# Kernel tuning notes

Measured on AMD Instinct MI355X. Metric: run time of the kernel, lower is better.

The kernel has to match this reference:

```python
import jax, jax.numpy as jnp
import numpy as np

L, D_IN, D_OUT, H = 4096, 512, 256, 4
HEAD = D_OUT // H  # 64


def setup_inputs() -> dict:
    key = jax.random.key(0)
    k1, k2, k3, k4, k5 = jax.random.split(key, 5)
    h = jax.random.normal(k1, (L, D_IN), dtype=jnp.float32)
    A = jax.random.randint(k2, (L, L), 0, 2, dtype=jnp.int32)
    W = jax.random.normal(k3, (D_OUT, D_IN), dtype=jnp.float32) * 0.05
    attn = jax.random.normal(k4, (H, 2 * HEAD), dtype=jnp.float32) * 0.05
    out_w = jax.random.normal(k5, (D_OUT, D_OUT), dtype=jnp.float32) * 0.05
    out_b = jnp.zeros((D_OUT,), dtype=jnp.float32)
    return {"h": h, "A": A, "W": W, "attn": attn, "out_w": out_w, "out_b": out_b}


def reference(h, A, W, attn, out_w, out_b):
    # h: (L, D_in), A: (L, L) in {0,1}
    Lq = h.shape[0]
    n_heads, two_d = attn.shape
    d = two_d // 2
    Wh = (h @ W.T).reshape(Lq, n_heads, d)  # (L, H, d)
    # Algebraic rewrite of concat-score: e_ij = a1.Wh_i + a2.Wh_j
    a1, a2 = attn[:, :d], attn[:, d:]
    s_i = jnp.einsum("lhd,hd->lh", Wh, a1)  # (L, H)
    s_j = jnp.einsum("lhd,hd->lh", Wh, a2)  # (L, H)
    e = jax.nn.leaky_relu(s_i[:, None, :] + s_j[None, :, :], negative_slope=0.2)  # (L, L, H)
    mask = (A > 0)[:, :, None]  # (L, L, 1)
    NEG = jnp.asarray(-1e30, e.dtype)
    e = jnp.where(mask, e, NEG)
    # stable masked softmax over j (axis=1); rows with no neighbors -> alpha = 0
    m = jnp.max(e, axis=1, keepdims=True)
    m = jnp.where(m > NEG / 2, m, 0.0)
    ex = jnp.where(mask, jnp.exp(e - m), 0.0)
    denom = jnp.sum(ex, axis=1, keepdims=True)
    alpha = ex / jnp.where(denom > 0, denom, 1.0)  # (L, L, H)
    # dropout is identity in eval mode
    out = jnp.einsum("ijh,jhd->ihd", alpha, Wh).reshape(Lq, n_heads * d)
    return out @ out_w.T + out_b
```

## Files before the change

kernel.cpp:

```cpp
#include <hip/hip_runtime.h>
#include <hip/hip_bf16.h>

#define L_    4096
#define DIN   512
#define DOUT  256
#define NH    4
#define HD    64
#define JW    128

typedef unsigned short u16;
typedef __attribute__((ext_vector_type(8))) short short8;
typedef __attribute__((ext_vector_type(4))) float floatx4;

__device__ __forceinline__ float bf2f(u16 u) {
  union { unsigned u32; float f; } v; v.u32 = ((unsigned)u) << 16; return v.f;
}
__device__ __forceinline__ u16 f2bf(float f) {
  union { float f; unsigned u; } v; v.f = f;
  unsigned r = v.u + 0x7fff + ((v.u >> 16) & 1);
  return (u16)(r >> 16);
}
__device__ __forceinline__ unsigned cvt2(float a, float b) {
  __hip_bfloat162 v = __float22bfloat162_rn(make_float2(a, b));
  return *reinterpret_cast<unsigned*>(&v);
}
__device__ __forceinline__ short8 pack8(const float* __restrict__ p) {
  float4 a = *(const float4*)p, b = *(const float4*)(p + 4);
  union { unsigned u[4]; short8 s; } r;
  r.u[0] = cvt2(a.x, a.y); r.u[1] = cvt2(a.z, a.w);
  r.u[2] = cvt2(b.x, b.y); r.u[3] = cvt2(b.z, b.w);
  return r.s;
}

__device__ __forceinline__ void mfma_cdmap(int lane, int* rowm, int* colm) {
  const int c0 = lane & 15;
  union { u16 u[8]; short8 s; } a1, b1, a2, b2;
  const u16 one = f2bf(1.f), cid = f2bf((float)c0);
  #pragma unroll
  for (int j = 0; j < 8; ++j) { a1.u[j] = cid; b1.u[j] = one; a2.u[j] = one; b2.u[j] = cid; }
  floatx4 z = {0.f, 0.f, 0.f, 0.f};
  floatx4 dr = __builtin_amdgcn_mfma_f32_16x16x32_bf16(a1.s, b1.s, z, 0, 0, 0);
  floatx4 dc = __builtin_amdgcn_mfma_f32_16x16x32_bf16(a2.s, b2.s, z, 0, 0, 0);
  #pragma unroll
  for (int r = 0; r < 4; ++r) {
    rowm[r] = (int)(dr[r] * 0.03125f + 0.5f);
    colm[r] = (int)(dc[r] * 0.03125f + 0.5f);
  }
}

__global__ __launch_bounds__(256) void k_ab(const int* __restrict__ A,
                                            unsigned* __restrict__ Abits,
                                            const float* __restrict__ W,
                                            u16* __restrict__ Wf) {
  const int t = threadIdx.x;
  const int g = blockIdx.x * 256 + t;
  const int lane = t & 63;
  #pragma unroll
  for (int r = 0; r < 8; ++r) {
    const size_t gi = (size_t)r * 524288 + g;
    int4 v = *(const int4*)(A + gi * 4);
    unsigned nib = (v.x > 0 ? 1u : 0u) | (v.y > 0 ? 2u : 0u)
                 | (v.z > 0 ? 4u : 0u) | (v.w > 0 ? 8u : 0u);
    unsigned part = nib << ((lane & 7) * 4);
    part |= __shfl_xor(part, 1, 64);
    part |= __shfl_xor(part, 2, 64);
    part |= __shfl_xor(part, 4, 64);
    if ((lane & 7) == 0) Abits[gi >> 3] = part;
  }
  if (blockIdx.x < 16) {
    const int col = g >> 4, kblock = g & 15;
    const int cg = col >> 6, nt = (col >> 4) & 3, c0 = col & 15;
    const float* src = W + (size_t)col * DIN + kblock * 32;
    u16* dst = Wf + ((size_t)(cg * 4 + nt) * 16 + kblock) * 512 + c0 * 8;
    #pragma unroll
    for (int q = 0; q < 4; ++q) {
      short8 v = pack8(src + q * 8);
      *(short8*)(dst + q * 128) = v;
    }
  }
}

__global__ __launch_bounds__(256) void k1_wh(
    const float* __restrict__ h, const u16* __restrict__ Wf,
    const float* __restrict__ attn,
    u16* __restrict__ WhTf, float* __restrict__ s1g, float2* __restrict__ bdg)
{
  const int i0 = blockIdx.x * 16;
  const int t = threadIdx.x;
  const int wv = t >> 6, lane = t & 63, q = lane >> 4, c0 = lane & 15;
  const int cg = wv;
  int rowm[4], colm[4];
  mfma_cdmap(lane, rowm, colm);

  __shared__ u16  hT[16][DIN + 8];
  __shared__ float pA[16][DOUT + 8];
  __shared__ float attnL[NH * 128];
  __shared__ float s1p[4][64];
  __shared__ float s2p[4][64];

  attnL[t] = attn[t];
  attnL[t + 256] = attn[t + 256];
  #pragma unroll
  for (int rep = 0; rep < 4; ++rep) {
    const int idx = rep * 256 + t;
    const int row = idx >> 6, c8 = (idx & 63) * 8;
    const float* hp = h + (size_t)(i0 + row) * DIN + c8;
    float4 a = *(const float4*)hp;
    float4 b = *(const float4*)(hp + 4);
    union { unsigned u[4]; int4 v; } pk;
    pk.u[0] = cvt2(a.x, a.y); pk.u[1] = cvt2(a.z, a.w);
    pk.u[2] = cvt2(b.x, b.y); pk.u[3] = cvt2(b.z, b.w);
    *(int4*)&hT[row][c8] = pk.v;
  }
  __syncthreads();

  floatx4 acc[4] = {};
  #pragma unroll
  for (int ks = 0; ks < 16; ++ks) {
    const int kb = ks * 32 + q * 8;
    short8 af = *(const short8*)&hT[c0][kb];
    #pragma unroll
    for (int nt = 0; nt < 4; ++nt) {
      short8 bf = *(const short8*)(Wf + ((size_t)(cg * 4 + nt) * 16 + ks) * 512 + lane * 8);
      acc[nt] = __builtin_amdgcn_mfma_f32_16x16x32_bf16(af, bf, acc[nt], 0, 0, 0);
    }
  }

  #pragma unroll
  for (int nt = 0; nt < 4; ++nt)
    #pragma unroll
    for (int r = 0; r < 4; ++r)
      pA[rowm[r]][cg * 64 + nt * 16 + colm[r]] = acc[nt][r];
  __syncthreads();

  {
    const int r = t & 15, hh = (t >> 4) & 3, qt = t >> 6;
    float s1 = 0.f, s2 = 0.f;
    #pragma unroll
    for (int dd = 0; dd < 16; ++dd) {
      const int d = qt * 16 + dd;
      float v = pA[r][hh * 64 + d];
      s1 += v * attnL[hh * 128 + d];
      s2 += v * attnL[hh * 128 + 64 + d];
    }
    s1p[qt][hh * 16 + r] = s1;
    s2p[qt][hh * 16 + r] = s2;
  }
  __syncthreads();
  if (t < 64) {
    const int r = t & 15, hh = t >> 4;
    float s1 = s1p[0][t] + s1p[1][t] + s1p[2][t] + s1p[3][t];
    float s2 = s2p[0][t] + s2p[1][t] + s2p[2][t] + s2p[3][t];
    s1g[hh * L_ + i0 + r] = s1;
    bdg[hh * L_ + i0 + r] = make_float2(__expf(s2), __expf(0.2f * s2));
  }

  {
    const int d = t;
    const int hd = d >> 6, nt = (d >> 4) & 3, dc0 = d & 15;
    const int jblock = i0 >> 5, qbase = (i0 & 31) >> 3;
    u16* base = WhTf + ((size_t)(hd * 4 + nt) * JW + jblock) * 512 + dc0 * 8;
    #pragma unroll
    for (int jh = 0; jh < 2; ++jh) {
      const int i = jh * 8;
      union { unsigned u[4]; int4 v; } pk;
      pk.u[0] = cvt2(pA[i + 0][d], pA[i + 1][d]);
      pk.u[1] = cvt2(pA[i + 2][d], pA[i + 3][d]);
      pk.u[2] = cvt2(pA[i + 4][d], pA[i + 5][d]);
      pk.u[3] = cvt2(pA[i + 6][d], pA[i + 7][d]);
      *(int4*)(base + (qbase + jh) * 128) = pk.v;
    }
  }
}

__global__ __launch_bounds__(1024) void k2_attn(
    const unsigned* __restrict__ Abits, const u16* __restrict__ WhTf,
    const float* __restrict__ s1g, const float2* __restrict__ bdg,
    const float* __restrict__ out_w, const float* __restrict__ out_b,
    float* __restrict__ out)
{
  const int i0 = blockIdx.x * 16;
  const int t = threadIdx.x;
  const int wv = t >> 6, lane = t & 63, q = lane >> 4, c0 = lane & 15;
  const int hd = wv & 3, jc = wv >> 2;

  __shared__ float pA[NH][16][HD + 4];
  __shared__ float pB[NH][16][HD + 4];
  __shared__ float dden[NH][4][16];
  __shared__ float rcpS[NH][16];
  __shared__ u16  CnL[16][DOUT + 8];
  __shared__ unsigned AbitL[16][JW + 2];

  {
    const int row = t >> 6, l = t & 63;
    uint2 w2 = *(const uint2*)&Abits[(size_t)(i0 + row) * JW + l * 2];
    AbitL[row][l * 2] = w2.x;
    AbitL[row][l * 2 + 1] = w2.y;
  }
  int rowm[4], colm[4];
  mfma_cdmap(lane, rowm, colm);
  __syncthreads();

  const float s1v = s1g[hd * L_ + i0 + c0];
  const float av = __expf(s1v);
  const float cv = __expf(0.2f * s1v);
  const float th = __expf(-s1v);
  const float2* bdh = bdg + (size_t)hd * L_;
  const u16* Wc = WhTf + (size_t)(hd * 4) * JW * 512 + (size_t)(jc * 32) * 512 + lane * 8;
  const int jbase = jc * 1024;

  floatx4 acc[4] = {};
  float dpart = 0.f;

  union PF { unsigned u[4]; short8 s; };

  auto issueV = [&](int kt, float4* v) {
    const float2* p = bdh + jbase + kt * 32 + q * 8;
    v[0] = *(const float4*)p;       v[1] = *(const float4*)(p + 2);
    v[2] = *(const float4*)(p + 4); v[3] = *(const float4*)(p + 6);
  };
  auto issueW = [&](int kt, short8* w) {
    #pragma unroll
    for (int nt = 0; nt < 4; ++nt)
      w[nt] = *(const short8*)(Wc + ((size_t)nt * JW + kt) * 512);
  };
  auto sm8 = [&](const float4* v, int kt, PF& pf) {
    const unsigned mb = (AbitL[c0][jc * 32 + kt] >> (q * 8)) & 0xffu;
    const float bb[8] = {v[0].x, v[0].z, v[1].x, v[1].z, v[2].x, v[2].z, v[3].x, v[3].z};
    const float dd[8] = {v[0].y, v[0].w, v[1].y, v[1].w, v[2].y, v[2].w, v[3].y, v[3].w};
    float ex[8];
    #pragma unroll
    for (int jj = 0; jj < 8; ++jj) {
      float p = (bb[jj] >= th) ? (av * bb[jj]) : (cv * dd[jj]);
      ex[jj] = ((mb >> jj) & 1u) ? p : 0.f;
      dpart += ex[jj];
    }
    pf.u[0] = cvt2(ex[0], ex[1]); pf.u[1] = cvt2(ex[2], ex[3]);
    pf.u[2] = cvt2(ex[4], ex[5]); pf.u[3] = cvt2(ex[6], ex[7]);
  };
  auto mfma4 = [&](PF& pf, const short8* w) {
    #pragma unroll
    for (int nt = 0; nt < 4; ++nt)
      acc[nt] = __builtin_amdgcn_mfma_f32_16x16x32_bf16(pf.s, w[nt], acc[nt], 0, 0, 0);
  };

  float4 vA[4], vB[4];
  short8 wA[4], wB[4];
  PF pfA, pfB;

  issueV(0, vA); issueW(0, wA);
  issueV(1, vB); issueW(1, wB);
  __builtin_amdgcn_sched_barrier(0);
  sm8(vA, 0, pfA);

  #pragma unroll 1
  for (int u = 0; u < 15; ++u) {
    const int kt = 2 * u;
    issueV(kt + 2, vA);
    __builtin_amdgcn_sched_barrier(0);
    sm8(vB, kt + 1, pfB);
    mfma4(pfA, wA);
    __builtin_amdgcn_sched_barrier(0);
    issueW(kt + 2, wA);
    issueV(kt + 3, vB);
    __builtin_amdgcn_sched_barrier(0);
    mfma4(pfB, wB);
    __builtin_amdgcn_sched_barrier(0);
    issueW(kt + 3, wB);
    sm8(vA, kt + 2, pfA);
    __builtin_amdgcn_sched_barrier(0);
  }
  mfma4(pfA, wA);
  sm8(vB, 31, pfB);
  mfma4(pfB, wB);

  dpart += __shfl_xor(dpart, 16, 64);
  dpart += __shfl_xor(dpart, 32, 64);
  if (lane < 16) dden[hd][jc][lane] = dpart;

  auto writeT = [&](float (*P)[HD + 4]) {
    #pragma unroll
    for (int nt = 0; nt < 4; ++nt)
      #pragma unroll
      for (int r = 0; r < 4; ++r)
        P[rowm[r]][nt * 16 + colm[r]] = acc[nt][r];
  };
  auto addB2A = [&]() {
    const int h2 = t >> 8, rem = t & 255, row = rem >> 4, d4 = (rem & 15) * 4;
    float4* a = (float4*)&pA[h2][row][d4];
    float4 bv = *(float4*)&pB[h2][row][d4];
    float4 av2 = *a;
    av2.x += bv.x; av2.y += bv.y; av2.z += bv.z; av2.w += bv.w;
    *a = av2;
  };

  if (jc == 0) writeT(pA[hd]);
  if (jc == 1) writeT(pB[hd]);
  __syncthreads();
  if (t < 64) {
    const int hh = t >> 4, r = t & 15;
    float den = dden[hh][0][r] + dden[hh][1][r] + dden[hh][2][r] + dden[hh][3][r];
    rcpS[hh][r] = (den > 0.f) ? (1.f / den) : 0.f;
  }
  addB2A();
  __syncthreads();
  if (jc == 2) writeT(pB[hd]);
  __syncthreads();
  addB2A();
  __syncthreads();
  if (jc == 3) writeT(pB[hd]);
  __syncthreads();
  addB2A();
  __syncthreads();

  {
    const int row = t >> 6, c4 = (t & 63) * 4;
    #pragma unroll
    for (int x = 0; x < 4; ++x) {
      const int col = c4 + x;
      const int hh = col >> 6, d = col & 63;
      CnL[row][col] = f2bf(pA[hh][row][d] * rcpS[hh][row]);
    }
  }
  __syncthreads();

  if (wv < 4) {
    const int cg = wv;
    floatx4 o[4] = {};
    #pragma unroll
    for (int kt = 0; kt < DOUT / 32; ++kt) {
      const int kb2 = kt * 32 + q * 8;
      short8 afr = *(const short8*)(&CnL[c0][kb2]);
      #pragma unroll
      for (int nt = 0; nt < 4; ++nt) {
        const int col = cg * 64 + nt * 16 + c0;
        short8 bfo = pack8(out_w + (size_t)col * DOUT + kb2);
        o[nt] = __builtin_amdgcn_mfma_f32_16x16x32_bf16(afr, bfo, o[nt], 0, 0, 0);
      }
    }
    #pragma unroll
    for (int nt = 0; nt < 4; ++nt)
      #pragma unroll
      for (int r = 0; r < 4; ++r) {
        const int col = cg * 64 + nt * 16 + colm[r];
        out[(size_t)(i0 + rowm[r]) * DOUT + col] = o[nt][r] + out_b[col];
      }
  }
}

extern "C" void kernel_launch(void* const* d_in, const int* in_sizes, int n_in,
                              void* d_out, int out_size, void* d_ws, size_t ws_size,
                              hipStream_t stream) {
  const float* h     = (const float*)d_in[0];
  const int*   A     = (const int*)d_in[1];
  const float* W     = (const float*)d_in[2];
  const float* attn  = (const float*)d_in[3];
  const float* out_w = (const float*)d_in[4];
  const float* out_b = (const float*)d_in[5];
  float* outp = (float*)d_out;

  const size_t WHTF_B  = (size_t)DOUT * L_ * 2;
  const size_t S1_B    = (size_t)NH * L_ * 4;
  const size_t BD_B    = (size_t)NH * L_ * 8;
  const size_t ABITS_B = (size_t)L_ * JW * 4;
  const size_t AB_OFF  = WHTF_B + S1_B + BD_B;

  u16*    WhTf = (u16*)d_ws;
  float*  s1g  = (float*)((char*)d_ws + WHTF_B);
  float2* bdg  = (float2*)((char*)d_ws + WHTF_B + S1_B);
  unsigned* Abits = (ws_size >= AB_OFF + ABITS_B)
                  ? (unsigned*)((char*)d_ws + AB_OFF)
                  : (unsigned*)((char*)d_out + 2097152);
  u16* Wf = (u16*)d_out;

  hipLaunchKernelGGL(k_ab, dim3(2048), dim3(256), 0, stream, A, Abits, W, Wf);
  hipLaunchKernelGGL(k1_wh, dim3(L_ / 16), dim3(256), 0, stream,
                     h, Wf, attn, WhTf, s1g, bdg);
  hipLaunchKernelGGL(k2_attn, dim3(L_ / 16), dim3(1024), 0, stream,
                     Abits, WhTf, s1g, bdg, out_w, out_b, outp);
}
```

Before: 153.7 us.

## Fuse three kernels into one persistent kernel with grid-wide atomic barrier

Merges the adjacency bit-packing, the Wh projection and the attention/output kernels into a single 1024-thread kernel. Each block packs its own 16 rows of A into shared memory, which removes the global Abits round trip. It also reads W directly with on-the-fly bf16 packing instead of a pre-swizzled copy. A spin-wait atomic grid barrier separates the projection phase from the attention phase, and shared memory is reused through a union. The barrier depends on all 256 blocks being co-resident, and the projection phase uses only a quarter of the threads while the other threads pack A.

```diff
diff --git a/kernel.cpp b/kernel.cpp
--- a/kernel.cpp
+++ b/kernel.cpp
@@ -12,9 +12,6 @@
 typedef __attribute__((ext_vector_type(8))) short short8;
 typedef __attribute__((ext_vector_type(4))) float floatx4;
 
-__device__ __forceinline__ float bf2f(u16 u) {
-  union { unsigned u32; float f; } v; v.u32 = ((unsigned)u) << 16; return v.f;
-}
 __device__ __forceinline__ u16 f2bf(float f) {
   union { float f; unsigned u; } v; v.f = f;
   unsigned r = v.u + 0x7fff + ((v.u >> 16) & 1);
@@ -48,160 +45,155 @@
   }
 }
 
-__global__ __launch_bounds__(256) void k_ab(const int* __restrict__ A,
-                                            unsigned* __restrict__ Abits,
-                                            const float* __restrict__ W,
-                                            u16* __restrict__ Wf) {
-  const int t = threadIdx.x;
-  const int g = blockIdx.x * 256 + t;
-  const int lane = t & 63;
-  #pragma unroll
-  for (int r = 0; r < 8; ++r) {
-    const size_t gi = (size_t)r * 524288 + g;
-    int4 v = *(const int4*)(A + gi * 4);
-    unsigned nib = (v.x > 0 ? 1u : 0u) | (v.y > 0 ? 2u : 0u)
-                 | (v.z > 0 ? 4u : 0u) | (v.w > 0 ? 8u : 0u);
-    unsigned part = nib << ((lane & 7) * 4);
-    part |= __shfl_xor(part, 1, 64);
-    part |= __shfl_xor(part, 2, 64);
-    part |= __shfl_xor(part, 4, 64);
-    if ((lane & 7) == 0) Abits[gi >> 3] = part;
-  }
-  if (blockIdx.x < 16) {
-    const int col = g >> 4, kblock = g & 15;
-    const int cg = col >> 6, nt = (col >> 4) & 3, c0 = col & 15;
-    const float* src = W + (size_t)col * DIN + kblock * 32;
-    u16* dst = Wf + ((size_t)(cg * 4 + nt) * 16 + kblock) * 512 + c0 * 8;
-    #pragma unroll
-    for (int q = 0; q < 4; ++q) {
-      short8 v = pack8(src + q * 8);
-      *(short8*)(dst + q * 128) = v;
-    }
-  }
-}
-
-__global__ __launch_bounds__(256) void k1_wh(
-    const float* __restrict__ h, const u16* __restrict__ Wf,
-    const float* __restrict__ attn,
-    u16* __restrict__ WhTf, float* __restrict__ s1g, float2* __restrict__ bdg)
+__global__ __launch_bounds__(1024) void mega(
+    const float* __restrict__ h, const int* __restrict__ A,
+    const float* __restrict__ W, const float* __restrict__ attn,
+    const float* __restrict__ out_w, const float* __restrict__ out_b,
+    float* __restrict__ out,
+    u16* __restrict__ WhTf, float2* __restrict__ bdg, int* __restrict__ syncp)
 {
   const int i0 = blockIdx.x * 16;
   const int t = threadIdx.x;
   const int wv = t >> 6, lane = t & 63, q = lane >> 4, c0 = lane & 15;
-  const int cg = wv;
+
+  union SMEM {
+    struct {
+      u16   hT[16][DIN + 8];
+      float pAk1[16][DOUT + 8];
+      float attnL[NH * 128];
+      float s1p[4][64];
+      float s2p[4][64];
+    } p1;
+    struct {
+      float pA[NH][16][HD + 4];
+      float pB[NH][16][HD + 4];
+      float dden[NH][4][16];
+      float rcpS[NH][16];
+      u16  CnL[16][DOUT + 8];
+    } p2;
+  };
+  __shared__ SMEM sm;
+  __shared__ unsigned AbitL[16][JW + 2];
+  __shared__ float s1L[64];
+
   int rowm[4], colm[4];
   mfma_cdmap(lane, rowm, colm);
 
-  __shared__ u16  hT[16][DIN + 8];
-  __shared__ float pA[16][DOUT + 8];
-  __shared__ float attnL[NH * 128];
-  __shared__ float s1p[4][64];
-  __shared__ float s2p[4][64];
-
-  attnL[t] = attn[t];
-  attnL[t + 256] = attn[t + 256];
-  #pragma unroll
-  for (int rep = 0; rep < 4; ++rep) {
-    const int idx = rep * 256 + t;
-    const int row = idx >> 6, c8 = (idx & 63) * 8;
-    const float* hp = h + (size_t)(i0 + row) * DIN + c8;
-    float4 a = *(const float4*)hp;
-    float4 b = *(const float4*)(hp + 4);
-    union { unsigned u[4]; int4 v; } pk;
-    pk.u[0] = cvt2(a.x, a.y); pk.u[1] = cvt2(a.z, a.w);
-    pk.u[2] = cvt2(b.x, b.y); pk.u[3] = cvt2(b.z, b.w);
-    *(int4*)&hT[row][c8] = pk.v;
-  }
-  __syncthreads();
-
-  floatx4 acc[4] = {};
-  #pragma unroll
-  for (int ks = 0; ks < 16; ++ks) {
-    const int kb = ks * 32 + q * 8;
-    short8 af = *(const short8*)&hT[c0][kb];
-    #pragma unroll
-    for (int nt = 0; nt < 4; ++nt) {
-      short8 bf = *(const short8*)(Wf + ((size_t)(cg * 4 + nt) * 16 + ks) * 512 + lane * 8);
-      acc[nt] = __builtin_amdgcn_mfma_f32_16x16x32_bf16(af, bf, acc[nt], 0, 0, 0);
-    }
-  }
-
-  #pragma unroll
-  for (int nt = 0; nt < 4; ++nt)
-    #pragma unroll
-    for (int r = 0; r < 4; ++r)
-      pA[rowm[r]][cg * 64 + nt * 16 + colm[r]] = acc[nt][r];
-  __syncthreads();
-
-  {
+  if (t < 256) {
+    sm.p1.attnL[t] = attn[t];
+    sm.p1.attnL[t + 256] = attn[t + 256];
+    #pragma unroll
+    for (int rep = 0; rep < 4; ++rep) {
+      const int idx = rep * 256 + t;
+      const int row = idx >> 6, c8 = (idx & 63) * 8;
+      const float* hp = h + (size_t)(i0 + row) * DIN + c8;
+      float4 a = *(const float4*)hp;
+      float4 b = *(const float4*)(hp + 4);
+      union { unsigned u[4]; int4 v; } pk;
+      pk.u[0] = cvt2(a.x, a.y); pk.u[1] = cvt2(a.z, a.w);
+      pk.u[2] = cvt2(b.x, b.y); pk.u[3] = cvt2(b.z, b.w);
+      *(int4*)&sm.p1.hT[row][c8] = pk.v;
+    }
+  } else {
+    const int u = t - 256;
+    #pragma unroll
+    for (int rep = 0; rep < 3; ++rep) {
+      const int w = u + rep * 768;
+      if (w < 2048) {
+        const int row = w >> 7, wI = w & 127;
+        const int* p = A + (size_t)(i0 + row) * L_ + wI * 32;
+        unsigned bits = 0u;
+        #pragma unroll
+        for (int wd = 0; wd < 8; ++wd) {
+          int4 v = *(const int4*)(p + wd * 4);
+          bits |= (v.x > 0 ? 1u : 0u) << (wd * 4 + 0);
+          bits |= (v.y > 0 ? 1u : 0u) << (wd * 4 + 1);
+          bits |= (v.z > 0 ? 1u : 0u) << (wd * 4 + 2);
+          bits |= (v.w > 0 ? 1u : 0u) << (wd * 4 + 3);
+        }
+        AbitL[row][wI] = bits;
+      }
+    }
+  }
+  __syncthreads();
+
+  if (t < 256) {
+    const int cg = wv;
+    floatx4 acc[4] = {};
+    #pragma unroll
+    for (int ks = 0; ks < 16; ++ks) {
+      const int kb = ks * 32 + q * 8;
+      short8 af = *(const short8*)&sm.p1.hT[c0][kb];
+      #pragma unroll
+      for (int nt = 0; nt < 4; ++nt) {
+        const int col = cg * 64 + nt * 16 + c0;
+        short8 bf = pack8(W + (size_t)col * DIN + kb);
+        acc[nt] = __builtin_amdgcn_mfma_f32_16x16x32_bf16(af, bf, acc[nt], 0, 0, 0);
+      }
+    }
+    #pragma unroll
+    for (int nt = 0; nt < 4; ++nt)
+      #pragma unroll
+      for (int r = 0; r < 4; ++r)
+        sm.p1.pAk1[rowm[r]][cg * 64 + nt * 16 + colm[r]] = acc[nt][r];
+  }
+  __syncthreads();
+
+  if (t < 256) {
     const int r = t & 15, hh = (t >> 4) & 3, qt = t >> 6;
     float s1 = 0.f, s2 = 0.f;
     #pragma unroll
     for (int dd = 0; dd < 16; ++dd) {
       const int d = qt * 16 + dd;
-      float v = pA[r][hh * 64 + d];
-      s1 += v * attnL[hh * 128 + d];
-      s2 += v * attnL[hh * 128 + 64 + d];
-    }
-    s1p[qt][hh * 16 + r] = s1;
-    s2p[qt][hh * 16 + r] = s2;
+      float v = sm.p1.pAk1[r][hh * 64 + d];
+      s1 += v * sm.p1.attnL[hh * 128 + d];
+      s2 += v * sm.p1.attnL[hh * 128 + 64 + d];
+    }
+    sm.p1.s1p[qt][hh * 16 + r] = s1;
+    sm.p1.s2p[qt][hh * 16 + r] = s2;
   }
   __syncthreads();
   if (t < 64) {
+    float s1 = sm.p1.s1p[0][t] + sm.p1.s1p[1][t] + sm.p1.s1p[2][t] + sm.p1.s1p[3][t];
+    float s2 = sm.p1.s2p[0][t] + sm.p1.s2p[1][t] + sm.p1.s2p[2][t] + sm.p1.s2p[3][t];
     const int r = t & 15, hh = t >> 4;
-    float s1 = s1p[0][t] + s1p[1][t] + s1p[2][t] + s1p[3][t];
-    float s2 = s2p[0][t] + s2p[1][t] + s2p[2][t] + s2p[3][t];
-    s1g[hh * L_ + i0 + r] = s1;
+    s1L[t] = s1;
     bdg[hh * L_ + i0 + r] = make_float2(__expf(s2), __expf(0.2f * s2));
   }
-
-  {
+  if (t < 256) {
     const int d = t;
-    const int hd = d >> 6, nt = (d >> 4) & 3, dc0 = d & 15;
+    const int hd2 = d >> 6, nt = (d >> 4) & 3, dc0 = d & 15;
     const int jblock = i0 >> 5, qbase = (i0 & 31) >> 3;
-    u16* base = WhTf + ((size_t)(hd * 4 + nt) * JW + jblock) * 512 + dc0 * 8;
+    u16* base = WhTf + ((size_t)(hd2 * 4 + nt) * JW + jblock) * 512 + dc0 * 8;
     #pragma unroll
     for (int jh = 0; jh < 2; ++jh) {
       const int i = jh * 8;
       union { unsigned u[4]; int4 v; } pk;
-      pk.u[0] = cvt2(pA[i + 0][d], pA[i + 1][d]);
-      pk.u[1] = cvt2(pA[i + 2][d], pA[i + 3][d]);
-      pk.u[2] = cvt2(pA[i + 4][d], pA[i + 5][d]);
-      pk.u[3] = cvt2(pA[i + 6][d], pA[i + 7][d]);
+      pk.u[0] = cvt2(sm.p1.pAk1[i + 0][d], sm.p1.pAk1[i + 1][d]);
+      pk.u[1] = cvt2(sm.p1.pAk1[i + 2][d], sm.p1.pAk1[i + 3][d]);
+      pk.u[2] = cvt2(sm.p1.pAk1[i + 4][d], sm.p1.pAk1[i + 5][d]);
+      pk.u[3] = cvt2(sm.p1.pAk1[i + 6][d], sm.p1.pAk1[i + 7][d]);
       *(int4*)(base + (qbase + jh) * 128) = pk.v;
     }
   }
-}
-
-__global__ __launch_bounds__(1024) void k2_attn(
-    const unsigned* __restrict__ Abits, const u16* __restrict__ WhTf,
-    const float* __restrict__ s1g, const float2* __restrict__ bdg,
-    const float* __restrict__ out_w, const float* __restrict__ out_b,
-    float* __restrict__ out)
-{
-  const int i0 = blockIdx.x * 16;
-  const int t = threadIdx.x;
-  const int wv = t >> 6, lane = t & 63, q = lane >> 4, c0 = lane & 15;
+
+  __syncthreads();
+  if (t == 0) {
+    int old = __hip_atomic_fetch_add(&syncp[0], 1, __ATOMIC_ACQ_REL,
+                                     __HIP_MEMORY_SCOPE_AGENT);
+    if (old == (int)gridDim.x - 1) {
+      __hip_atomic_store(&syncp[1], 1, __ATOMIC_RELEASE,
+                         __HIP_MEMORY_SCOPE_AGENT);
+    } else {
+      while (__hip_atomic_load(&syncp[1], __ATOMIC_ACQUIRE,
+                               __HIP_MEMORY_SCOPE_AGENT) == 0)
+        __builtin_amdgcn_s_sleep(2);
+    }
+  }
+  __syncthreads();
+
   const int hd = wv & 3, jc = wv >> 2;
-
-  __shared__ float pA[NH][16][HD + 4];
-  __shared__ float pB[NH][16][HD + 4];
-  __shared__ float dden[NH][4][16];
-  __shared__ float rcpS[NH][16];
-  __shared__ u16  CnL[16][DOUT + 8];
-  __shared__ unsigned AbitL[16][JW + 2];
-
-  {
-    const int row = t >> 6, l = t & 63;
-    uint2 w2 = *(const uint2*)&Abits[(size_t)(i0 + row) * JW + l * 2];
-    AbitL[row][l * 2] = w2.x;
-    AbitL[row][l * 2 + 1] = w2.y;
-  }
-  int rowm[4], colm[4];
-  mfma_cdmap(lane, rowm, colm);
-  __syncthreads();
-
-  const float s1v = s1g[hd * L_ + i0 + c0];
+  const float s1v = s1L[hd * 16 + c0];
   const float av = __expf(s1v);
   const float cv = __expf(0.2f * s1v);
   const float th = __expf(-s1v);
@@ -254,8 +246,8 @@
   sm8(vA, 0, pfA);
 
   #pragma unroll 1
-  for (int u = 0; u < 15; ++u) {
-    const int kt = 2 * u;
+  for (int u2 = 0; u2 < 15; ++u2) {
+    const int kt = 2 * u2;
     issueV(kt + 2, vA);
     __builtin_amdgcn_sched_barrier(0);
     sm8(vB, kt + 1, pfB);
@@ -276,7 +268,7 @@
 
   dpart += __shfl_xor(dpart, 16, 64);
   dpart += __shfl_xor(dpart, 32, 64);
-  if (lane < 16) dden[hd][jc][lane] = dpart;
+  if (lane < 16) sm.p2.dden[hd][jc][lane] = dpart;
 
   auto writeT = [&](float (*P)[HD + 4]) {
     #pragma unroll
@@ -287,28 +279,29 @@
   };
   auto addB2A = [&]() {
     const int h2 = t >> 8, rem = t & 255, row = rem >> 4, d4 = (rem & 15) * 4;
-    float4* a = (float4*)&pA[h2][row][d4];
-    float4 bv = *(float4*)&pB[h2][row][d4];
+    float4* a = (float4*)&sm.p2.pA[h2][row][d4];
+    float4 bv = *(float4*)&sm.p2.pB[h2][row][d4];
     float4 av2 = *a;
     av2.x += bv.x; av2.y += bv.y; av2.z += bv.z; av2.w += bv.w;
     *a = av2;
   };
 
-  if (jc == 0) writeT(pA[hd]);
-  if (jc == 1) writeT(pB[hd]);
+  if (jc == 0) writeT(sm.p2.pA[hd]);
+  if (jc == 1) writeT(sm.p2.pB[hd]);
   __syncthreads();
   if (t < 64) {
     const int hh = t >> 4, r = t & 15;
-    float den = dden[hh][0][r] + dden[hh][1][r] + dden[hh][2][r] + dden[hh][3][r];
-    rcpS[hh][r] = (den > 0.f) ? (1.f / den) : 0.f;
+    float den = sm.p2.dden[hh][0][r] + sm.p2.dden[hh][1][r]
+              + sm.p2.dden[hh][2][r] + sm.p2.dden[hh][3][r];
+    sm.p2.rcpS[hh][r] = (den > 0.f) ? (1.f / den) : 0.f;
   }
   addB2A();
   __syncthreads();
-  if (jc == 2) writeT(pB[hd]);
+  if (jc == 2) writeT(sm.p2.pB[hd]);
   __syncthreads();
   addB2A();
   __syncthreads();
-  if (jc == 3) writeT(pB[hd]);
+  if (jc == 3) writeT(sm.p2.pB[hd]);
   __syncthreads();
   addB2A();
   __syncthreads();
@@ -319,7 +312,7 @@
     for (int x = 0; x < 4; ++x) {
       const int col = c4 + x;
       const int hh = col >> 6, d = col & 63;
-      CnL[row][col] = f2bf(pA[hh][row][d] * rcpS[hh][row]);
+      sm.p2.CnL[row][col] = f2bf(sm.p2.pA[hh][row][d] * sm.p2.rcpS[hh][row]);
     }
   }
   __syncthreads();
@@ -330,7 +323,7 @@
     #pragma unroll
     for (int kt = 0; kt < DOUT / 32; ++kt) {
       const int kb2 = kt * 32 + q * 8;
-      short8 afr = *(const short8*)(&CnL[c0][kb2]);
+      short8 afr = *(const short8*)(&sm.p2.CnL[c0][kb2]);
       #pragma unroll
       for (int nt = 0; nt < 4; ++nt) {
         const int col = cg * 64 + nt * 16 + c0;
@@ -359,23 +352,13 @@
   const float* out_b = (const float*)d_in[5];
   float* outp = (float*)d_out;
 
-  const size_t WHTF_B  = (size_t)DOUT * L_ * 2;
-  const size_t S1_B    = (size_t)NH * L_ * 4;
-  const size_t BD_B    = (size_t)NH * L_ * 8;
-  const size_t ABITS_B = (size_t)L_ * JW * 4;
-  const size_t AB_OFF  = WHTF_B + S1_B + BD_B;
-
-  u16*    WhTf = (u16*)d_ws;
-  float*  s1g  = (float*)((char*)d_ws + WHTF_B);
-  float2* bdg  = (float2*)((char*)d_ws + WHTF_B + S1_B);
-  unsigned* Abits = (ws_size >= AB_OFF + ABITS_B)
-                  ? (unsigned*)((char*)d_ws + AB_OFF)
-                  : (unsigned*)((char*)d_out + 2097152);
-  u16* Wf = (u16*)d_out;
-
-  hipLaunchKernelGGL(k_ab, dim3(2048), dim3(256), 0, stream, A, Abits, W, Wf);
-  hipLaunchKernelGGL(k1_wh, dim3(L_ / 16), dim3(256), 0, stream,
-                     h, Wf, attn, WhTf, s1g, bdg);
-  hipLaunchKernelGGL(k2_attn, dim3(L_ / 16), dim3(1024), 0, stream,
-                     Abits, WhTf, s1g, bdg, out_w, out_b, outp);
-}
+  const size_t WHTF_B = (size_t)DOUT * L_ * 2;
+  const size_t BD_B   = (size_t)NH * L_ * 8;
+  u16*    WhTf  = (u16*)d_ws;
+  float2* bdg   = (float2*)((char*)d_ws + WHTF_B);
+  int*    syncp = (int*)((char*)d_ws + WHTF_B + BD_B);
+
+  hipMemsetAsync(syncp, 0, 2 * sizeof(int), stream);
+  hipLaunchKernelGGL(mega, dim3(L_ / 16), dim3(1024), 0, stream,
+                     h, A, W, attn, out_w, out_b, outp, WhTf, bdg, syncp);
+}
```

New measurement: 203.0 us. 1.32x slower.
